# Performance work log

Measured on AMD Instinct MI355X. Metric: run time of the kernel, lower is better.

The kernel has to match this reference:

```python
import jax, jax.numpy as jnp
import numpy as np

N_NODES = 100000
N_EDGES = 1600000
D_IN, D_HID, N_CLS = 256, 128, 47


def setup_inputs() -> dict:
    key = jax.random.key(0)
    k = jax.random.split(key, 5)
    x = jax.random.normal(k[0], (N_NODES, D_IN), dtype=jnp.float32)
    edge_index = jax.random.randint(k[1], (2, N_EDGES), 0, N_NODES, dtype=jnp.int64)
    W1 = jax.random.normal(k[2], (D_IN, D_HID), dtype=jnp.float32) * 0.05
    b1 = jnp.zeros((D_HID,), dtype=jnp.float32)
    W2 = jax.random.normal(k[3], (D_HID, N_CLS), dtype=jnp.float32) * 0.05
    b2 = jnp.zeros((N_CLS,), dtype=jnp.float32)
    return {"x": x, "edge_index": edge_index, "W1": W1, "b1": b1, "W2": W2, "b2": b2}


def _gcn_conv(x, W, b, src, dst, norm, n):
    # PyG GCNConv: linear transform, normalized scatter-add aggregation, bias after
    h = x @ W                                   # [N, D_out]
    msg = h[src] * norm[:, None]                # gather over edges [E', D_out]
    agg = jax.ops.segment_sum(msg, dst, num_segments=n)
    return agg + b


def reference(x, edge_index, W1, b1, W2, b2):
    n = x.shape[0]
    loop = jnp.arange(n, dtype=edge_index.dtype)
    src = jnp.concatenate([edge_index[0], loop])  # add self-loops
    dst = jnp.concatenate([edge_index[1], loop])
    # symmetric normalization D^-1/2 (A+I) D^-1/2 (degree = in-degree incl. self-loop)
    deg = jax.ops.segment_sum(jnp.ones_like(dst, dtype=x.dtype), dst, num_segments=n)
    dinv = jnp.where(deg > 0, jax.lax.rsqrt(deg), 0.0)
    norm = dinv[src] * dinv[dst]                 # [E']
    h1 = jax.nn.relu(_gcn_conv(x, W1, b1, src, dst, norm, n))
    # dropout with training=False is identity
    out = _gcn_conv(h1, W2, b2, src, dst, norm, n)
    return out
```

## Files before the change

kernel.cpp:

```cpp
#include <hip/hip_runtime.h>
#include <hip/hip_bf16.h>

#define DIN 256
#define DHID 128
#define NCLS 47
#define BSHIFT 9
#define BNODES 512
#define NPART 256
#define BCAPS 9216
#define CHUNKE 6400

typedef __attribute__((ext_vector_type(8))) short short8;
typedef __attribute__((ext_vector_type(4))) float f32x4;

__device__ __forceinline__ short f2bf(float f) {
    __bf16 b = (__bf16)f;
    return __builtin_bit_cast(short, b);
}
__device__ __forceinline__ float bfu(unsigned int u) {
    return __uint_as_float(u << 16);
}
__device__ __forceinline__ float bfh(unsigned int u) {
    return __uint_as_float(u & 0xffff0000u);
}
__device__ __forceinline__ unsigned int pack2(float lo, float hi) {
    return (unsigned int)(unsigned short)f2bf(lo)
         | ((unsigned int)(unsigned short)f2bf(hi) << 16);
}
__device__ __forceinline__ void add8(float* a, uint4 v) {
    a[0] += bfu(v.x); a[1] += bfh(v.x);
    a[2] += bfu(v.y); a[3] += bfh(v.y);
    a[4] += bfu(v.z); a[5] += bfh(v.z);
    a[6] += bfu(v.w); a[7] += bfh(v.w);
}
__device__ __forceinline__ void fma8(float* a, uint4 v, float d) {
    a[0] += d * bfu(v.x); a[1] += d * bfh(v.x);
    a[2] += d * bfu(v.y); a[3] += d * bfh(v.y);
    a[4] += d * bfu(v.z); a[5] += d * bfh(v.z);
    a[6] += d * bfu(v.w); a[7] += d * bfh(v.w);
}

__global__ __launch_bounds__(256) void k_prep_hist(const float* __restrict__ W1,
                                                   const float* __restrict__ W2,
                                                   short* __restrict__ W1s,
                                                   short* __restrict__ W2s,
                                                   const int* __restrict__ dst,
                                                   int* __restrict__ ghist,
                                                   int E, int NB, int chunk) {
    __shared__ int lh[256];
    int blk = blockIdx.x, t = threadIdx.x;
    if (blk < 16) {
        int tid = blk * 256 + t;
        int frag = tid >> 6, lane = tid & 63;
        int kt = frag >> 3, nt = frag & 7;
        int quad = lane >> 4, col = lane & 15;
        #pragma unroll
        for (int j = 0; j < 8; ++j) {
            int k = kt * 32 + quad * 8 + j;
            W1s[(size_t)tid * 8 + j] = f2bf(W1[k * DHID + nt * 16 + col]);
        }
    } else if (blk < 20) {
        int tid = (blk - 16) * 256 + t;
        int frag = tid >> 6, lane = tid & 63;
        int kt = frag >> 2, nt = frag & 3;
        int quad = lane >> 4, col = lane & 15;
        int c = nt * 16 + col;
        #pragma unroll
        for (int j = 0; j < 8; ++j) {
            int k = kt * 32 + quad * 8 + j;
            float v = (c < NCLS) ? W2[k * NCLS + c] : 0.0f;
            W2s[(size_t)tid * 8 + j] = f2bf(v);
        }
    } else {
        int p = blk - 20;
        for (int i = t; i < NB; i += 256) lh[i] = 0;
        __syncthreads();
        int lo = p * chunk, hi = min(E, lo + chunk);
        for (int i = lo + t; i < hi; i += 256)
            atomicAdd(&lh[dst[i] >> BSHIFT], 1);
        __syncthreads();
        for (int i = t; i < NB; i += 256) ghist[(size_t)i * NPART + p] = lh[i];
    }
}

__global__ __launch_bounds__(256) void k_scatter_gemm1(const int* __restrict__ src,
                                                       const int* __restrict__ dst,
                                                       const int* __restrict__ ghist,
                                                       int* __restrict__ btot,
                                                       unsigned int* __restrict__ bbuf,
                                                       int E, int NB, int chunk,
                                                       const float* __restrict__ x,
                                                       const short* __restrict__ W1s,
                                                       short* __restrict__ hb, int n) {
    __shared__ __align__(16) char smem[65536];
    int blk = blockIdx.x, t = threadIdx.x;

    if (blk < NPART) {
        unsigned int* stage = (unsigned int*)smem;
        int* sdest = (int*)(smem + 25600);
        int* lcur  = (int*)(smem + 51200);
        int* gdst  = (int*)(smem + 52224);
        int* wsum  = (int*)(smem + 53248);

        int tot = 0, pref = 0, mine = 0;
        if (t < NB) {
            const int* gp = ghist + (size_t)t * NPART;
            mine = gp[blk];
            #pragma unroll 8
            for (int p = 0; p < NPART; ++p) {
                int v = gp[p];
                tot += v;
                pref += (p < blk) ? v : 0;
            }
        }
        if (blk == 0 && t < NB) btot[t] = tot;

        int lane = t & 63, w = t >> 6;
        int incl = tot;
        #pragma unroll
        for (int off = 1; off < 64; off <<= 1) {
            int u = __shfl_up(incl, off, 64);
            if (lane >= off) incl += u;
        }
        if (lane == 63) wsum[w] = incl;
        __syncthreads();
        int wadd = 0;
        for (int i = 0; i < w; ++i) wadd += wsum[i];
        int bbase = wadd + incl - tot;
        __syncthreads();
        incl = mine;
        #pragma unroll
        for (int off = 1; off < 64; off <<= 1) {
            int u = __shfl_up(incl, off, 64);
            if (lane >= off) incl += u;
        }
        if (lane == 63) wsum[w] = incl;
        __syncthreads();
        wadd = 0;
        for (int i = 0; i < w; ++i) wadd += wsum[i];
        int ex = wadd + incl - mine;

        lcur[t] = ex;
        gdst[t] = bbase + pref - ex;
        __syncthreads();

        int lo = blk * chunk, hi = min(E, lo + chunk), cnt = hi - lo;
        for (int i = lo + t; i < hi; i += 256) {
            int d = dst[i];
            int b = d >> BSHIFT;
            int slot = atomicAdd(&lcur[b], 1);
            stage[slot] = (unsigned int)src[i] | ((unsigned int)(d & (BNODES - 1)) << 17);
            sdest[slot] = gdst[b] + slot;
        }
        __syncthreads();
        for (int i = t; i < cnt; i += 256)
            bbuf[sdest[i]] = stage[i];
    } else {
        short* lw = (short*)smem;
        {
            const uint4* g = (const uint4*)W1s;
            uint4* l = (uint4*)lw;
            for (int i = t; i < 4096; i += 256) l[i] = g[i];
        }
        __syncthreads();

        int bid = blk - NPART;
        int wave = t >> 6, lane = t & 63;
        int quad = lane >> 4, lrow = lane & 15;
        long long rowbase = (long long)bid * 128 + wave * 32;

        f32x4 acc[2][8];
        #pragma unroll
        for (int rt = 0; rt < 2; ++rt)
            #pragma unroll
            for (int nt = 0; nt < 8; ++nt) acc[rt][nt] = (f32x4){0.f, 0.f, 0.f, 0.f};

        const short8* lf = (const short8*)lw;

        #pragma unroll
        for (int kt = 0; kt < 8; ++kt) {
            int k0 = kt * 32 + quad * 8;
            short8 a[2];
            #pragma unroll
            for (int rt = 0; rt < 2; ++rt) {
                long long row = rowbase + rt * 16 + lrow;
                float4 v0 = {0.f,0.f,0.f,0.f}, v1 = {0.f,0.f,0.f,0.f};
                if (row < n) {
                    const float* xp = x + row * DIN + k0;
                    v0 = *(const float4*)xp;
                    v1 = *(const float4*)(xp + 4);
                }
                short8 av;
                av[0] = f2bf(v0.x); av[1] = f2bf(v0.y); av[2] = f2bf(v0.z); av[3] = f2bf(v0.w);
                av[4] = f2bf(v1.x); av[5] = f2bf(v1.y); av[6] = f2bf(v1.z); av[7] = f2bf(v1.w);
                a[rt] = av;
            }
            #pragma unroll
            for (int nt = 0; nt < 8; ++nt) {
                short8 b = lf[(kt * 8 + nt) * 64 + lane];
                acc[0][nt] = __builtin_amdgcn_mfma_f32_16x16x32_bf16(a[0], b, acc[0][nt], 0, 0, 0);
                acc[1][nt] = __builtin_amdgcn_mfma_f32_16x16x32_bf16(a[1], b, acc[1][nt], 0, 0, 0);
            }
        }
        #pragma unroll
        for (int rt = 0; rt < 2; ++rt)
            #pragma unroll
            for (int nt = 0; nt < 8; ++nt)
                #pragma unroll
                for (int r = 0; r < 4; ++r) {
                    long long row = rowbase + rt * 16 + quad * 4 + r;
                    if (row < n) hb[row * DHID + nt * 16 + lrow] = f2bf(acc[rt][nt][r]);
                }
    }
}

__device__ __forceinline__ void scan_btot(const int* __restrict__ btot, int NB,
                                          int* lbase, int* wsum) {
    int t = threadIdx.x;
    int v = (t < NB) ? btot[t] : 0;
    int incl = v;
    int lane = t & 63, w = t >> 6;
    #pragma unroll
    for (int off = 1; off < 64; off <<= 1) {
        int u = __shfl_up(incl, off, 64);
        if (lane >= off) incl += u;
    }
    if (lane == 63) wsum[w] = incl;
    __syncthreads();
    int wadd = 0;
    for (int i = 0; i < w; ++i) wadd += wsum[i];
    lbase[t] = wadd + incl - v;
    __syncthreads();
}

__global__ __launch_bounds__(256) void k_bsort(const int* __restrict__ btot,
                                               unsigned int* __restrict__ bbuf,
                                               int* __restrict__ degi,
                                               int* __restrict__ beg,
                                               float* __restrict__ dinv, int n, int NB) {
    __shared__ unsigned int stage[BCAPS];
    __shared__ int hist[BNODES];
    __shared__ int cur[BNODES];
    __shared__ int lbase[256];
    __shared__ int wsum[4];

    int b = blockIdx.x, t = threadIdx.x;
    scan_btot(btot, NB, lbase, wsum);
    int cnt = min(btot[b], BCAPS);
    int gbase = lbase[b];
    int node0 = b << BSHIFT;

    if (t < 128) { ((int2*)hist)[t] = (int2){0, 0}; ((int2*)hist)[t + 128] = (int2){0, 0}; }
    __syncthreads();

    for (int i = t; i < cnt; i += 256) {
        unsigned int p = bbuf[gbase + i];
        stage[i] = p;
        atomicAdd(&hist[p >> 17], 1);
    }
    __syncthreads();

    int v0 = hist[2 * t], v1 = hist[2 * t + 1];
    int s = v0 + v1;
    int incl = s;
    int lane = t & 63, w = t >> 6;
    #pragma unroll
    for (int off = 1; off < 64; off <<= 1) {
        int u = __shfl_up(incl, off, 64);
        if (lane >= off) incl += u;
    }
    if (lane == 63) wsum[w] = incl;
    __syncthreads();
    int wadd = 0;
    for (int i = 0; i < w; ++i) wadd += wsum[i];
    int ex = wadd + incl - s;
    cur[2 * t] = ex;
    cur[2 * t + 1] = ex + v0;
    int nodeA = node0 + 2 * t, nodeB = node0 + 2 * t + 1;
    if (nodeA < n) {
        degi[nodeA] = v0;
        beg[nodeA]  = gbase + ex;
        dinv[nodeA] = rsqrtf((float)(v0 + 1));
    }
    if (nodeB < n) {
        degi[nodeB] = v1;
        beg[nodeB]  = gbase + ex + v0;
        dinv[nodeB] = rsqrtf((float)(v1 + 1));
    }
    __syncthreads();

    for (int i = t; i < cnt; i += 256) {
        unsigned int p = stage[i];
        int slot = atomicAdd(&cur[p >> 17], 1);
        bbuf[gbase + slot] = p & 0x1FFFFu;
    }
}

__global__ __launch_bounds__(256) void k_gather1(const int* __restrict__ beg,
                          const int* __restrict__ degi,
                          const int* __restrict__ ssrc, const float* __restrict__ dinv,
                          const uint4* __restrict__ hb4, const float* __restrict__ b1,
                          uint4* __restrict__ h1u4, int n) {
    int node = blockIdx.x * 4 + (threadIdx.x >> 6);
    int t = threadIdx.x & 63;
    if (node >= n) return;
    int cnt = degi[node];
    int bg  = beg[node];
    int grp = t >> 4, sub = t & 15;

    float a[8] = {0.f,0.f,0.f,0.f,0.f,0.f,0.f,0.f};
    int k = 0;
    for (; k + 16 <= cnt; k += 16) {
        int s[4];
        #pragma unroll
        for (int q = 0; q < 4; ++q) s[q] = ssrc[bg + k + grp * 4 + q];
        float dv[4]; uint4 v[4];
        #pragma unroll
        for (int q = 0; q < 4; ++q) { dv[q] = dinv[s[q]]; v[q] = hb4[(size_t)s[q] * 16 + sub]; }
        #pragma unroll
        for (int q = 0; q < 4; ++q) fma8(a, v[q], dv[q]);
    }
    for (; k < cnt; k += 4) {
        int idx = k + grp;
        if (idx < cnt) {
            int s = ssrc[bg + idx];
            fma8(a, hb4[(size_t)s * 16 + sub], dinv[s]);
        }
    }

    #pragma unroll
    for (int j = 0; j < 8; ++j) {
        a[j] += __shfl_xor(a[j], 16);
        a[j] += __shfl_xor(a[j], 32);
    }

    if (grp == 0) {
        uint4 sv = hb4[(size_t)node * 16 + sub];
        float di = dinv[node], dd = di * di;
        float4 bA = ((const float4*)b1)[sub * 2];
        float4 bB = ((const float4*)b1)[sub * 2 + 1];
        float v0 = fmaxf(di * a[0] + dd * bfu(sv.x) + bA.x, 0.f);
        float v1 = fmaxf(di * a[1] + dd * bfh(sv.x) + bA.y, 0.f);
        float v2 = fmaxf(di * a[2] + dd * bfu(sv.y) + bA.z, 0.f);
        float v3 = fmaxf(di * a[3] + dd * bfh(sv.y) + bA.w, 0.f);
        float v4 = fmaxf(di * a[4] + dd * bfu(sv.z) + bB.x, 0.f);
        float v5 = fmaxf(di * a[5] + dd * bfh(sv.z) + bB.y, 0.f);
        float v6 = fmaxf(di * a[6] + dd * bfu(sv.w) + bB.z, 0.f);
        float v7 = fmaxf(di * a[7] + dd * bfh(sv.w) + bB.w, 0.f);
        uint4 o;
        o.x = pack2(v0, v1);
        o.y = pack2(v2, v3);
        o.z = pack2(v4, v5);
        o.w = pack2(v6, v7);
        h1u4[(size_t)node * 16 + sub] = o;
    }
}

__global__ __launch_bounds__(256) void k_gemm2_mfma(const short* __restrict__ h1b,
                                                    const short* __restrict__ W2s,
                                                    const float* __restrict__ dinv,
                                                    short* __restrict__ h2b, int n) {
    __shared__ short lw[8192];
    {
        const uint4* g = (const uint4*)W2s;
        uint4* l = (uint4*)lw;
        for (int i = threadIdx.x; i < 1024; i += 256) l[i] = g[i];
    }
    __syncthreads();

    int wave = threadIdx.x >> 6, lane = threadIdx.x & 63;
    int quad = lane >> 4, lrow = lane & 15;
    long long row0 = (long long)blockIdx.x * 64 + wave * 16;

    f32x4 acc[4];
    #pragma unroll
    for (int nt = 0; nt < 4; ++nt) acc[nt] = (f32x4){0.f, 0.f, 0.f, 0.f};

    const short8* lf = (const short8*)lw;

    #pragma unroll
    for (int kt = 0; kt < 4; ++kt) {
        long long row = row0 + lrow;
        short8 a = (short8){0,0,0,0,0,0,0,0};
        if (row < n) a = *(const short8*)(h1b + row * DHID + kt * 32 + quad * 8);
        #pragma unroll
        for (int nt = 0; nt < 4; ++nt)
            acc[nt] = __builtin_amdgcn_mfma_f32_16x16x32_bf16(a, lf[(kt * 4 + nt) * 64 + lane], acc[nt], 0, 0, 0);
    }
    float dvv[4];
    #pragma unroll
    for (int r = 0; r < 4; ++r) {
        long long row = row0 + quad * 4 + r;
        dvv[r] = (row < n) ? dinv[row] : 0.f;
    }
    #pragma unroll
    for (int nt = 0; nt < 4; ++nt)
        #pragma unroll
        for (int r = 0; r < 4; ++r) {
            long long row = row0 + quad * 4 + r;
            if (row < n) h2b[row * 64 + nt * 16 + lrow] = f2bf(acc[nt][r] * dvv[r]);
        }
}

__global__ __launch_bounds__(256) void k_gather2(const int* __restrict__ beg,
                          const int* __restrict__ degi,
                          const int* __restrict__ ssrc, const float* __restrict__ dinv,
                          const uint4* __restrict__ h2b4, const float* __restrict__ b2,
                          float* __restrict__ out, int n) {
    int node = blockIdx.x * 4 + (threadIdx.x >> 6);
    int t = threadIdx.x & 63;
    if (node >= n) return;
    int cnt = degi[node];
    int bg  = beg[node];
    int grp = t >> 3, sub = t & 7;

    float a[8] = {0.f,0.f,0.f,0.f,0.f,0.f,0.f,0.f};
    int k = 0;
    for (; k + 16 <= cnt; k += 16) {
        int s0 = ssrc[bg + k + grp], s1 = ssrc[bg + k + 8 + grp];
        uint4 v0 = h2b4[(size_t)s0 * 8 + sub];
        uint4 v1 = h2b4[(size_t)s1 * 8 + sub];
        add8(a, v0); add8(a, v1);
    }
    for (; k < cnt; k += 8) {
        int idx = k + grp;
        if (idx < cnt) {
            int s = ssrc[bg + idx];
            add8(a, h2b4[(size_t)s * 8 + sub]);
        }
    }
    if (grp == 0) add8(a, h2b4[(size_t)node * 8 + sub]);

    #pragma unroll
    for (int j = 0; j < 8; ++j) {
        a[j] += __shfl_xor(a[j], 8);
        a[j] += __shfl_xor(a[j], 16);
        a[j] += __shfl_xor(a[j], 32);
    }

    if (grp == 0) {
        float di = dinv[node];
        #pragma unroll
        for (int j = 0; j < 8; ++j) {
            int c = sub * 8 + j;
            if (c < NCLS) out[(size_t)node * NCLS + c] = di * a[j] + b2[c];
        }
    }
}

extern "C" void kernel_launch(void* const* d_in, const int* in_sizes, int n_in,
                              void* d_out, int out_size, void* d_ws, size_t ws_size,
                              hipStream_t stream) {
    const float* x  = (const float*)d_in[0];
    const int*   ei = (const int*)d_in[1];
    const float* W1 = (const float*)d_in[2];
    const float* b1 = (const float*)d_in[3];
    const float* W2 = (const float*)d_in[4];
    const float* b2 = (const float*)d_in[5];

    const int n = in_sizes[0] / DIN;
    const int E = in_sizes[1] / 2;
    const int* src = ei;
    const int* dst = ei + E;
    float* out = (float*)d_out;

    const int NB = (n + BNODES - 1) >> BSHIFT;
    const int chunk = (E + NPART - 1) / NPART;

    char* w = (char*)d_ws;
    int*   ghist = (int*)w;                    w += (size_t)NB * NPART * 4;
    int*   btot  = (int*)w;                    w += ((size_t)NB * 4 + 15) & ~15ull;
    int*   degi  = (int*)w;                    w += (size_t)n * 4;
    int*   beg   = (int*)w;                    w += (size_t)n * 4;
    float* dinv  = (float*)w;                  w += (size_t)n * 4;
    short* W1s   = (short*)w;                  w += (size_t)32768 * 2;
    short* W2s   = (short*)w;                  w += (size_t)8192 * 2;
    unsigned int* bbuf = (unsigned int*)w;     w += (size_t)E * 4;
    short* hb    = (short*)w;                  w += (size_t)n * DHID * 2;
    short* h1b   = (short*)w;                  w += (size_t)n * DHID * 2;
    short* h2b   = (short*)w;                  w += (size_t)n * 64 * 2;

    k_prep_hist<<<20 + NPART, 256, 0, stream>>>(W1, W2, W1s, W2s, dst, ghist, E, NB, chunk);
    k_scatter_gemm1<<<NPART + (n + 127) / 128, 256, 0, stream>>>(src, dst, ghist, btot, bbuf,
                                                                 E, NB, chunk, x, W1s, hb, n);
    k_bsort<<<NB, 256, 0, stream>>>(btot, bbuf, degi, beg, dinv, n, NB);
    k_gather1<<<(n + 3) / 4, 256, 0, stream>>>(beg, degi, (const int*)bbuf, dinv,
                                               (const uint4*)hb, b1,
                                               (uint4*)h1b, n);
    k_gemm2_mfma<<<(n + 63) / 64, 256, 0, stream>>>(h1b, W2s, dinv, h2b, n);
    k_gather2<<<(n + 3) / 4, 256, 0, stream>>>(beg, degi, (const int*)bbuf, dinv,
                                               (const uint4*)h2b, b2, out, n);
}
```

Before: 402.6 us.

## Replace bucketed two-pass CSR sort with global-atomic degree count and direct scatter

The CSR build drops the per-partition histogram, bucket staging scatter and per-bucket LDS sort. It now counts per-node in-degree with global atomics, computes offsets with a block scan fused into the gemm1 launch, then scatters source indices straight into place through per-node atomic cursors. The layer-2 feature buffer also shrinks from 64 to 48 bf16 columns per node, cutting MFMA tiles and gather bytes. In exchange, global atomic contention on degc and cur goes up, the edge order within a node becomes nondeterministic, and a memset plus an extra launch are added.

```diff
diff --git a/kernel.cpp b/kernel.cpp
--- a/kernel.cpp
+++ b/kernel.cpp
@@ -6,9 +6,6 @@
 #define NCLS 47
 #define BSHIFT 9
 #define BNODES 512
-#define NPART 256
-#define BCAPS 9216
-#define CHUNKE 6400
 
 typedef __attribute__((ext_vector_type(8))) short short8;
 typedef __attribute__((ext_vector_type(4))) float f32x4;
@@ -40,14 +37,13 @@
     a[6] += d * bfu(v.w); a[7] += d * bfh(v.w);
 }
 
-__global__ __launch_bounds__(256) void k_prep_hist(const float* __restrict__ W1,
-                                                   const float* __restrict__ W2,
-                                                   short* __restrict__ W1s,
-                                                   short* __restrict__ W2s,
-                                                   const int* __restrict__ dst,
-                                                   int* __restrict__ ghist,
-                                                   int E, int NB, int chunk) {
-    __shared__ int lh[256];
+__global__ __launch_bounds__(256) void k_prep(const float* __restrict__ W1,
+                                              const float* __restrict__ W2,
+                                              short* __restrict__ W1s,
+                                              short* __restrict__ W2s,
+                                              const int* __restrict__ dst,
+                                              int* __restrict__ degc,
+                                              int* __restrict__ btot, int E) {
     int blk = blockIdx.x, t = threadIdx.x;
     if (blk < 16) {
         int tid = blk * 256 + t;
@@ -72,51 +68,71 @@
             W2s[(size_t)tid * 8 + j] = f2bf(v);
         }
     } else {
+        __shared__ int lh[256];
+        lh[t] = 0;
+        __syncthreads();
         int p = blk - 20;
-        for (int i = t; i < NB; i += 256) lh[i] = 0;
+        int e4 = E >> 2;
+        int idx = p * 256 + t;
+        if (idx < e4) {
+            int4 d4 = ((const int4*)dst)[idx];
+            atomicAdd(&degc[d4.x], 1);  atomicAdd(&lh[d4.x >> BSHIFT], 1);
+            atomicAdd(&degc[d4.y], 1);  atomicAdd(&lh[d4.y >> BSHIFT], 1);
+            atomicAdd(&degc[d4.z], 1);  atomicAdd(&lh[d4.z >> BSHIFT], 1);
+            atomicAdd(&degc[d4.w], 1);  atomicAdd(&lh[d4.w >> BSHIFT], 1);
+        }
+        if (p == 0 && t < (E & 3)) {
+            int d = dst[(e4 << 2) + t];
+            atomicAdd(&degc[d], 1);  atomicAdd(&lh[d >> BSHIFT], 1);
+        }
         __syncthreads();
-        int lo = p * chunk, hi = min(E, lo + chunk);
-        for (int i = lo + t; i < hi; i += 256)
-            atomicAdd(&lh[dst[i] >> BSHIFT], 1);
-        __syncthreads();
-        for (int i = t; i < NB; i += 256) ghist[(size_t)i * NPART + p] = lh[i];
-    }
-}
-
-__global__ __launch_bounds__(256) void k_scatter_gemm1(const int* __restrict__ src,
-                                                       const int* __restrict__ dst,
-                                                       const int* __restrict__ ghist,
-                                                       int* __restrict__ btot,
-                                                       unsigned int* __restrict__ bbuf,
-                                                       int E, int NB, int chunk,
-                                                       const float* __restrict__ x,
-                                                       const short* __restrict__ W1s,
-                                                       short* __restrict__ hb, int n) {
+        if (lh[t]) atomicAdd(&btot[t], lh[t]);
+    }
+}
+
+__device__ __forceinline__ void scan_btot(const int* __restrict__ btot, int NB,
+                                          int* lbase, int* wsum) {
+    int t = threadIdx.x;
+    int v = (t < NB) ? btot[t] : 0;
+    int incl = v;
+    int lane = t & 63, w = t >> 6;
+    #pragma unroll
+    for (int off = 1; off < 64; off <<= 1) {
+        int u = __shfl_up(incl, off, 64);
+        if (lane >= off) incl += u;
+    }
+    if (lane == 63) wsum[w] = incl;
+    __syncthreads();
+    int wadd = 0;
+    for (int i = 0; i < w; ++i) wadd += wsum[i];
+    lbase[t] = wadd + incl - v;
+    __syncthreads();
+}
+
+__global__ __launch_bounds__(256) void k_build_gemm1(const int* __restrict__ btot,
+                                                     const int* __restrict__ degc,
+                                                     int* __restrict__ degi,
+                                                     int* __restrict__ beg,
+                                                     int* __restrict__ cur,
+                                                     float* __restrict__ dinv,
+                                                     int n, int NB,
+                                                     const float* __restrict__ x,
+                                                     const short* __restrict__ W1s,
+                                                     short* __restrict__ hb) {
     __shared__ __align__(16) char smem[65536];
     int blk = blockIdx.x, t = threadIdx.x;
 
-    if (blk < NPART) {
-        unsigned int* stage = (unsigned int*)smem;
-        int* sdest = (int*)(smem + 25600);
-        int* lcur  = (int*)(smem + 51200);
-        int* gdst  = (int*)(smem + 52224);
-        int* wsum  = (int*)(smem + 53248);
-
-        int tot = 0, pref = 0, mine = 0;
-        if (t < NB) {
-            const int* gp = ghist + (size_t)t * NPART;
-            mine = gp[blk];
-            #pragma unroll 8
-            for (int p = 0; p < NPART; ++p) {
-                int v = gp[p];
-                tot += v;
-                pref += (p < blk) ? v : 0;
-            }
-        }
-        if (blk == 0 && t < NB) btot[t] = tot;
-
+    if (blk < NB) {
+        int* lbase = (int*)smem;
+        int* wsum  = (int*)(smem + 1024);
+        scan_btot(btot, NB, lbase, wsum);
+        int base = lbase[blk];
+        int node0 = blk << BSHIFT;
+        int i0 = node0 + 2 * t;
+        int v0 = degc[i0], v1 = degc[i0 + 1];
+        int s = v0 + v1;
+        int incl = s;
         int lane = t & 63, w = t >> 6;
-        int incl = tot;
         #pragma unroll
         for (int off = 1; off < 64; off <<= 1) {
             int u = __shfl_up(incl, off, 64);
@@ -126,35 +142,19 @@
         __syncthreads();
         int wadd = 0;
         for (int i = 0; i < w; ++i) wadd += wsum[i];
-        int bbase = wadd + incl - tot;
-        __syncthreads();
-        incl = mine;
-        #pragma unroll
-        for (int off = 1; off < 64; off <<= 1) {
-            int u = __shfl_up(incl, off, 64);
-            if (lane >= off) incl += u;
-        }
-        if (lane == 63) wsum[w] = incl;
-        __syncthreads();
-        wadd = 0;
-        for (int i = 0; i < w; ++i) wadd += wsum[i];
-        int ex = wadd + incl - mine;
-
-        lcur[t] = ex;
-        gdst[t] = bbase + pref - ex;
-        __syncthreads();
-
-        int lo = blk * chunk, hi = min(E, lo + chunk), cnt = hi - lo;
-        for (int i = lo + t; i < hi; i += 256) {
-            int d = dst[i];
-            int b = d >> BSHIFT;
-            int slot = atomicAdd(&lcur[b], 1);
-            stage[slot] = (unsigned int)src[i] | ((unsigned int)(d & (BNODES - 1)) << 17);
-            sdest[slot] = gdst[b] + slot;
-        }
-        __syncthreads();
-        for (int i = t; i < cnt; i += 256)
-            bbuf[sdest[i]] = stage[i];
+        int ex = wadd + incl - s;
+        if (i0 < n) {
+            degi[i0] = v0;
+            beg[i0]  = base + ex;
+            cur[i0]  = base + ex;
+            dinv[i0] = rsqrtf((float)(v0 + 1));
+        }
+        if (i0 + 1 < n) {
+            degi[i0 + 1] = v1;
+            beg[i0 + 1]  = base + ex + v0;
+            cur[i0 + 1]  = base + ex + v0;
+            dinv[i0 + 1] = rsqrtf((float)(v1 + 1));
+        }
     } else {
         short* lw = (short*)smem;
         {
@@ -164,7 +164,7 @@
         }
         __syncthreads();
 
-        int bid = blk - NPART;
+        int bid = blk - NB;
         int wave = t >> 6, lane = t & 63;
         int quad = lane >> 4, lrow = lane & 15;
         long long rowbase = (long long)bid * 128 + wave * 32;
@@ -214,85 +214,23 @@
     }
 }
 
-__device__ __forceinline__ void scan_btot(const int* __restrict__ btot, int NB,
-                                          int* lbase, int* wsum) {
-    int t = threadIdx.x;
-    int v = (t < NB) ? btot[t] : 0;
-    int incl = v;
-    int lane = t & 63, w = t >> 6;
-    #pragma unroll
-    for (int off = 1; off < 64; off <<= 1) {
-        int u = __shfl_up(incl, off, 64);
-        if (lane >= off) incl += u;
-    }
-    if (lane == 63) wsum[w] = incl;
-    __syncthreads();
-    int wadd = 0;
-    for (int i = 0; i < w; ++i) wadd += wsum[i];
-    lbase[t] = wadd + incl - v;
-    __syncthreads();
-}
-
-__global__ __launch_bounds__(256) void k_bsort(const int* __restrict__ btot,
-                                               unsigned int* __restrict__ bbuf,
-                                               int* __restrict__ degi,
-                                               int* __restrict__ beg,
-                                               float* __restrict__ dinv, int n, int NB) {
-    __shared__ unsigned int stage[BCAPS];
-    __shared__ int hist[BNODES];
-    __shared__ int cur[BNODES];
-    __shared__ int lbase[256];
-    __shared__ int wsum[4];
-
-    int b = blockIdx.x, t = threadIdx.x;
-    scan_btot(btot, NB, lbase, wsum);
-    int cnt = min(btot[b], BCAPS);
-    int gbase = lbase[b];
-    int node0 = b << BSHIFT;
-
-    if (t < 128) { ((int2*)hist)[t] = (int2){0, 0}; ((int2*)hist)[t + 128] = (int2){0, 0}; }
-    __syncthreads();
-
-    for (int i = t; i < cnt; i += 256) {
-        unsigned int p = bbuf[gbase + i];
-        stage[i] = p;
-        atomicAdd(&hist[p >> 17], 1);
-    }
-    __syncthreads();
-
-    int v0 = hist[2 * t], v1 = hist[2 * t + 1];
-    int s = v0 + v1;
-    int incl = s;
-    int lane = t & 63, w = t >> 6;
-    #pragma unroll
-    for (int off = 1; off < 64; off <<= 1) {
-        int u = __shfl_up(incl, off, 64);
-        if (lane >= off) incl += u;
-    }
-    if (lane == 63) wsum[w] = incl;
-    __syncthreads();
-    int wadd = 0;
-    for (int i = 0; i < w; ++i) wadd += wsum[i];
-    int ex = wadd + incl - s;
-    cur[2 * t] = ex;
-    cur[2 * t + 1] = ex + v0;
-    int nodeA = node0 + 2 * t, nodeB = node0 + 2 * t + 1;
-    if (nodeA < n) {
-        degi[nodeA] = v0;
-        beg[nodeA]  = gbase + ex;
-        dinv[nodeA] = rsqrtf((float)(v0 + 1));
-    }
-    if (nodeB < n) {
-        degi[nodeB] = v1;
-        beg[nodeB]  = gbase + ex + v0;
-        dinv[nodeB] = rsqrtf((float)(v1 + 1));
-    }
-    __syncthreads();
-
-    for (int i = t; i < cnt; i += 256) {
-        unsigned int p = stage[i];
-        int slot = atomicAdd(&cur[p >> 17], 1);
-        bbuf[gbase + slot] = p & 0x1FFFFu;
+__global__ __launch_bounds__(256) void k_scatter(const int* __restrict__ src,
+                                                 const int* __restrict__ dst,
+                                                 int* __restrict__ cur,
+                                                 int* __restrict__ bbuf, int E) {
+    int idx = blockIdx.x * 256 + threadIdx.x;
+    int e4 = E >> 2;
+    if (idx < e4) {
+        int4 s4 = ((const int4*)src)[idx];
+        int4 d4 = ((const int4*)dst)[idx];
+        bbuf[atomicAdd(&cur[d4.x], 1)] = s4.x;
+        bbuf[atomicAdd(&cur[d4.y], 1)] = s4.y;
+        bbuf[atomicAdd(&cur[d4.z], 1)] = s4.z;
+        bbuf[atomicAdd(&cur[d4.w], 1)] = s4.w;
+    }
+    if (blockIdx.x == 0 && threadIdx.x < (E & 3)) {
+        int i = (e4 << 2) + threadIdx.x;
+        bbuf[atomicAdd(&cur[dst[i]], 1)] = src[i];
     }
 }
 
@@ -372,9 +310,9 @@
     int quad = lane >> 4, lrow = lane & 15;
     long long row0 = (long long)blockIdx.x * 64 + wave * 16;
 
-    f32x4 acc[4];
-    #pragma unroll
-    for (int nt = 0; nt < 4; ++nt) acc[nt] = (f32x4){0.f, 0.f, 0.f, 0.f};
+    f32x4 acc[3];
+    #pragma unroll
+    for (int nt = 0; nt < 3; ++nt) acc[nt] = (f32x4){0.f, 0.f, 0.f, 0.f};
 
     const short8* lf = (const short8*)lw;
 
@@ -384,7 +322,7 @@
         short8 a = (short8){0,0,0,0,0,0,0,0};
         if (row < n) a = *(const short8*)(h1b + row * DHID + kt * 32 + quad * 8);
         #pragma unroll
-        for (int nt = 0; nt < 4; ++nt)
+        for (int nt = 0; nt < 3; ++nt)
             acc[nt] = __builtin_amdgcn_mfma_f32_16x16x32_bf16(a, lf[(kt * 4 + nt) * 64 + lane], acc[nt], 0, 0, 0);
     }
     float dvv[4];
@@ -394,18 +332,18 @@
         dvv[r] = (row < n) ? dinv[row] : 0.f;
     }
     #pragma unroll
-    for (int nt = 0; nt < 4; ++nt)
+    for (int nt = 0; nt < 3; ++nt)
         #pragma unroll
         for (int r = 0; r < 4; ++r) {
             long long row = row0 + quad * 4 + r;
-            if (row < n) h2b[row * 64 + nt * 16 + lrow] = f2bf(acc[nt][r] * dvv[r]);
+            if (row < n) h2b[row * 48 + nt * 16 + lrow] = f2bf(acc[nt][r] * dvv[r]);
         }
 }
 
 __global__ __launch_bounds__(256) void k_gather2(const int* __restrict__ beg,
                           const int* __restrict__ degi,
                           const int* __restrict__ ssrc, const float* __restrict__ dinv,
-                          const uint4* __restrict__ h2b4, const float* __restrict__ b2,
+                          const uint4* __restrict__ h2b6, const float* __restrict__ b2,
                           float* __restrict__ out, int n) {
     int node = blockIdx.x * 4 + (threadIdx.x >> 6);
     int t = threadIdx.x & 63;
@@ -418,18 +356,20 @@
     int k = 0;
     for (; k + 16 <= cnt; k += 16) {
         int s0 = ssrc[bg + k + grp], s1 = ssrc[bg + k + 8 + grp];
-        uint4 v0 = h2b4[(size_t)s0 * 8 + sub];
-        uint4 v1 = h2b4[(size_t)s1 * 8 + sub];
-        add8(a, v0); add8(a, v1);
+        if (sub < 6) {
+            uint4 v0 = h2b6[(size_t)s0 * 6 + sub];
+            uint4 v1 = h2b6[(size_t)s1 * 6 + sub];
+            add8(a, v0); add8(a, v1);
+        }
     }
     for (; k < cnt; k += 8) {
         int idx = k + grp;
         if (idx < cnt) {
             int s = ssrc[bg + idx];
-            add8(a, h2b4[(size_t)s * 8 + sub]);
-        }
-    }
-    if (grp == 0) add8(a, h2b4[(size_t)node * 8 + sub]);
+            if (sub < 6) add8(a, h2b6[(size_t)s * 6 + sub]);
+        }
+    }
+    if (grp == 0 && sub < 6) add8(a, h2b6[(size_t)node * 6 + sub]);
 
     #pragma unroll
     for (int j = 0; j < 8; ++j) {
@@ -465,29 +405,34 @@
     float* out = (float*)d_out;
 
     const int NB = (n + BNODES - 1) >> BSHIFT;
-    const int chunk = (E + NPART - 1) / NPART;
+    const int npad = NB << BSHIFT;
 
     char* w = (char*)d_ws;
-    int*   ghist = (int*)w;                    w += (size_t)NB * NPART * 4;
-    int*   btot  = (int*)w;                    w += ((size_t)NB * 4 + 15) & ~15ull;
-    int*   degi  = (int*)w;                    w += (size_t)n * 4;
-    int*   beg   = (int*)w;                    w += (size_t)n * 4;
-    float* dinv  = (float*)w;                  w += (size_t)n * 4;
-    short* W1s   = (short*)w;                  w += (size_t)32768 * 2;
-    short* W2s   = (short*)w;                  w += (size_t)8192 * 2;
-    unsigned int* bbuf = (unsigned int*)w;     w += (size_t)E * 4;
-    short* hb    = (short*)w;                  w += (size_t)n * DHID * 2;
-    short* h1b   = (short*)w;                  w += (size_t)n * DHID * 2;
-    short* h2b   = (short*)w;                  w += (size_t)n * 64 * 2;
-
-    k_prep_hist<<<20 + NPART, 256, 0, stream>>>(W1, W2, W1s, W2s, dst, ghist, E, NB, chunk);
-    k_scatter_gemm1<<<NPART + (n + 127) / 128, 256, 0, stream>>>(src, dst, ghist, btot, bbuf,
-                                                                 E, NB, chunk, x, W1s, hb, n);
-    k_bsort<<<NB, 256, 0, stream>>>(btot, bbuf, degi, beg, dinv, n, NB);
-    k_gather1<<<(n + 3) / 4, 256, 0, stream>>>(beg, degi, (const int*)bbuf, dinv,
+    int*   degc = (int*)w;                     w += (size_t)npad * 4;
+    int*   btot = (int*)w;                     w += (size_t)256 * 4;
+    int*   degi = (int*)w;                     w += (size_t)n * 4;
+    int*   beg  = (int*)w;                     w += (size_t)n * 4;
+    int*   cur  = (int*)w;                     w += (size_t)n * 4;
+    float* dinv = (float*)w;                   w += (size_t)n * 4;
+    short* W1s  = (short*)w;                   w += (size_t)32768 * 2;
+    short* W2s  = (short*)w;                   w += (size_t)8192 * 2;
+    int*   bbuf = (int*)w;                     w += (size_t)E * 4;
+    short* hb   = (short*)w;                   w += (size_t)n * DHID * 2;
+    short* h1b  = (short*)w;                   w += (size_t)n * DHID * 2;
+    short* h2b  = (short*)w;                   w += (size_t)n * 48 * 2;
+
+    const int ndeg = (E + 1023) / 1024;
+    const int nsc  = ((E >> 2) + 255) / 256;
+
+    hipMemsetAsync(degc, 0, ((size_t)npad + 256) * 4, stream);
+    k_prep<<<20 + ndeg, 256, 0, stream>>>(W1, W2, W1s, W2s, dst, degc, btot, E);
+    k_build_gemm1<<<NB + (n + 127) / 128, 256, 0, stream>>>(btot, degc, degi, beg, cur,
+                                                            dinv, n, NB, x, W1s, hb);
+    k_scatter<<<nsc, 256, 0, stream>>>(src, dst, cur, bbuf, E);
+    k_gather1<<<(n + 3) / 4, 256, 0, stream>>>(beg, degi, bbuf, dinv,
                                                (const uint4*)hb, b1,
                                                (uint4*)h1b, n);
     k_gemm2_mfma<<<(n + 63) / 64, 256, 0, stream>>>(h1b, W2s, dinv, h2b, n);
-    k_gather2<<<(n + 3) / 4, 256, 0, stream>>>(beg, degi, (const int*)bbuf, dinv,
+    k_gather2<<<(n + 3) / 4, 256, 0, stream>>>(beg, degi, bbuf, dinv,
                                                (const uint4*)h2b, b2, out, n);
 }
```

Measured after the change: 545.4 us. 1.35x slower.
